# Optimization experiments

Hardware: AMD Instinct MI355X
Metric: run time of the kernel (lower is better)

## Reference

```python
import jax, jax.numpy as jnp
import numpy as np

N = 20000      # nodes
E = 320000     # edges (before self-loops)
F_IN = 512     # input feature size
HID = 128      # encoder hidden
OUT = 128      # encoder output / GAT in_channels
H = 4          # gat heads
C = 64         # gat out_channels per head


def setup_inputs() -> dict:
    key = jax.random.key(0)
    ks = jax.random.split(key, 10)
    s = 0.05
    return {
        "x": jax.random.normal(ks[0], (N, F_IN), jnp.float32),
        "edge_index": jax.random.randint(ks[1], (2, E), 0, N, dtype=jnp.int64),
        "W1": jax.random.normal(ks[2], (F_IN, HID), jnp.float32) * s,
        "b1": jax.random.normal(ks[3], (HID,), jnp.float32) * s,
        "W2": jax.random.normal(ks[4], (HID, OUT), jnp.float32) * s,
        "b2": jax.random.normal(ks[5], (OUT,), jnp.float32) * s,
        "Wg": jax.random.normal(ks[6], (OUT, H * C), jnp.float32) * s,
        "att_src": jax.random.normal(ks[7], (H, C), jnp.float32) * s,
        "att_dst": jax.random.normal(ks[8], (H, C), jnp.float32) * s,
        "bias_g": jax.random.normal(ks[9], (H * C,), jnp.float32) * s,
    }


def reference(x, edge_index, W1, b1, W2, b2, Wg, att_src, att_dst, bias_g):
    # MLP encoder: Linear -> ReLU -> Linear
    h = jnp.maximum(x @ W1 + b1, 0.0) @ W2 + b2            # [N, OUT]

    # GATConv (concat=True, eval mode -> no dropout)
    xg = (h @ Wg).reshape(N, H, C)                          # per-head projections

    # add self-loops (PyG GATConv default)
    loops = jnp.arange(N, dtype=edge_index.dtype)
    src = jnp.concatenate([edge_index[0], loops])           # [E+N] source j
    dst = jnp.concatenate([edge_index[1], loops])           # [E+N] dest   i

    a_src = jnp.einsum('nhc,hc->nh', xg, att_src)           # [N, H]
    a_dst = jnp.einsum('nhc,hc->nh', xg, att_dst)           # [N, H]

    e = jax.nn.leaky_relu(a_src[src] + a_dst[dst], 0.2)     # [E+N, H]

    # segment softmax over incoming edges of each destination node
    m = jax.ops.segment_max(e, dst, num_segments=N)         # [N, H]
    ex = jnp.exp(e - m[dst])
    denom = jax.ops.segment_sum(ex, dst, num_segments=N)
    alpha = ex / (denom[dst] + 1e-16)                       # [E+N, H]

    # weighted scatter-add aggregation
    out = jax.ops.segment_sum(alpha[:, :, None] * xg[src], dst, num_segments=N)  # [N, H, C]
    return out.reshape(N, H * C) + bias_g
```

## Files before the change

kernel.cpp:

```cpp
#include <hip/hip_runtime.h>
#include <math.h>

#define NNODES 20000
#define NEDGES 320000
#define FIN    512
#define HIDD   128
#define OUTD   128
#define NH     4
#define NC     64
#define HC     256

typedef short bf16x8 __attribute__((ext_vector_type(8)));
typedef float f32x4  __attribute__((ext_vector_type(4)));

__device__ __forceinline__ unsigned short f2bf(float f) {
    unsigned int u = __float_as_uint(f);
    unsigned int r = 0x7fffu + ((u >> 16) & 1u);
    return (unsigned short)((u + r) >> 16);
}
__device__ __forceinline__ float bflo(unsigned int u) {
    return __uint_as_float(u << 16);
}
__device__ __forceinline__ float bfhi(unsigned int u) {
    return __uint_as_float(u & 0xffff0000u);
}

#define PREP_TB1 64
#define PREP_TB2 192
__global__ __launch_bounds__(256)
void prep_count_kernel(const float* __restrict__ W1, unsigned short* __restrict__ W1t,
                       const float* __restrict__ W2, const float* __restrict__ b2,
                       const float* __restrict__ Wg, unsigned short* __restrict__ W2gt,
                       float* __restrict__ b2g,
                       const int* __restrict__ e_dst, int* __restrict__ deg, int E) {
    const int bid = blockIdx.x;
    const int tid = threadIdx.x;
    if (bid < PREP_TB1) {
        __shared__ float tile[32][33];
        const int tk = bid >> 2;
        const int tn = bid & 3;
        const int k0 = tk * 32, n0 = tn * 32;
        const int nin = tid & 31;
        const int r8  = tid >> 5;
        #pragma unroll
        for (int s = 0; s < 4; ++s) {
            int k = s * 8 + r8;
            tile[k][nin] = W1[(size_t)(k0 + k) * HIDD + n0 + nin];
        }
        __syncthreads();
        #pragma unroll
        for (int s = 0; s < 4; ++s) {
            int nn = s * 8 + r8;
            W1t[(size_t)(n0 + nn) * FIN + k0 + nin] = f2bf(tile[nin][nn]);
        }
    } else if (bid < PREP_TB2) {
        int local = (bid - PREP_TB1) * 256 + tid;
        int nn = local >> 7;
        int k  = local & 127;
        float s = 0.f;
        #pragma unroll 8
        for (int t = 0; t < HIDD; ++t)
            s += W2[(size_t)k * OUTD + t] * Wg[(size_t)t * HC + nn];
        W2gt[(size_t)nn * HIDD + k] = f2bf(s);
        if (k == 0) {
            float t2 = 0.f;
            #pragma unroll 8
            for (int t = 0; t < OUTD; ++t) t2 += b2[t] * Wg[(size_t)t * HC + nn];
            b2g[nn] = t2;
        }
    } else {
        int i = (bid - PREP_TB2) * 256 + tid;
        if (i < E) atomicAdd(&deg[e_dst[i]], 1);
    }
}

__global__ __launch_bounds__(256)
void gemm1_kernel(const float* __restrict__ A,
                  const unsigned short* __restrict__ Bt,
                  const float* __restrict__ bias,
                  unsigned short* __restrict__ C, int M) {
    __shared__ unsigned short As[32 * 64];
    __shared__ unsigned short Bs[128 * 64];

    const int tid  = threadIdx.x;
    const int lane = tid & 63;
    const int w    = tid >> 6;
    const int wr   = w >> 1;
    const int wc   = w & 1;
    const int m0   = blockIdx.x * 32;

    char* pA = (char*)As;
    char* pB = (char*)Bs;

    f32x4 acc[4];
    #pragma unroll
    for (int n = 0; n < 4; ++n) acc[n] = (f32x4){0.f, 0.f, 0.f, 0.f};

    for (int k0 = 0; k0 < FIN; k0 += 64) {
        {
            const int row = tid >> 3;
            const int sg  = tid & 7;
            const bool ok = (m0 + row) < M;
            const float4* Ap = (const float4*)(A + (size_t)(m0 + row) * FIN + k0 + sg * 8);
            float4 f0 = make_float4(0,0,0,0), f1 = f0;
            if (ok) { f0 = Ap[0]; f1 = Ap[1]; }
            unsigned short u[8];
            u[0]=f2bf(f0.x); u[1]=f2bf(f0.y); u[2]=f2bf(f0.z); u[3]=f2bf(f0.w);
            u[4]=f2bf(f1.x); u[5]=f2bf(f1.y); u[6]=f2bf(f1.z); u[7]=f2bf(f1.w);
            *(bf16x8*)(pA + (((row * 128 + sg * 16)) ^ ((row & 7) << 4))) = *(bf16x8*)&u[0];
        }
        #pragma unroll
        for (int i = 0; i < 4; ++i) {
            int s   = tid + i * 256;
            int col = s >> 3;
            int sg  = s & 7;
            bf16x8 v = *(const bf16x8*)(Bt + (size_t)col * FIN + k0 + sg * 8);
            *(bf16x8*)(pB + (((col * 128 + sg * 16)) ^ ((col & 7) << 4))) = v;
        }
        __syncthreads();

        #pragma unroll
        for (int ks = 0; ks < 2; ++ks) {
            const int kb = ks * 64 + ((lane >> 4) << 4);
            int row = wr * 16 + (lane & 15);
            bf16x8 a = *(const bf16x8*)(pA + ((row * 128 + kb) ^ ((row & 7) << 4)));
            bf16x8 b[4];
            #pragma unroll
            for (int n = 0; n < 4; ++n) {
                int col = wc * 64 + n * 16 + (lane & 15);
                b[n] = *(const bf16x8*)(pB + ((col * 128 + kb) ^ ((col & 7) << 4)));
            }
            #pragma unroll
            for (int n = 0; n < 4; ++n)
                acc[n] = __builtin_amdgcn_mfma_f32_16x16x32_bf16(a, b[n], acc[n], 0, 0, 0);
        }
        __syncthreads();
    }

    #pragma unroll
    for (int n = 0; n < 4; ++n) {
        const int col = wc * 64 + n * 16 + (lane & 15);
        const float bv = bias[col];
        #pragma unroll
        for (int r = 0; r < 4; ++r) {
            const int row = m0 + wr * 16 + ((lane >> 4) << 2) + r;
            if (row >= M) continue;
            float v = fmaxf(acc[n][r] + bv, 0.f);
            C[(size_t)row * HIDD + col] = f2bf(v);
        }
    }
}

__global__ __launch_bounds__(1024)
void scan_offsets_kernel(const int* __restrict__ deg, int* __restrict__ offs,
                         int* __restrict__ cursor, unsigned short* __restrict__ csr16,
                         int n) {
    __shared__ int wsum[16], wbase[16];
    const int tid = threadIdx.x, lane = tid & 63, w = tid >> 6;
    const int i0 = tid * 20;
    int loc[20];
    int s = 0;
    #pragma unroll
    for (int k = 0; k < 20; ++k) {
        int i = i0 + k;
        int v = (i < n) ? (deg[i] + 1) : 0;
        loc[k] = s;
        s += v;
    }
    int incl = s;
    #pragma unroll
    for (int d = 1; d < 64; d <<= 1) {
        int t = __shfl_up(incl, d);
        if (lane >= d) incl += t;
    }
    if (lane == 63) wsum[w] = incl;
    __syncthreads();
    if (w == 0) {
        int v = (lane < 16) ? wsum[lane] : 0;
        int sc = v;
        #pragma unroll
        for (int d = 1; d < 16; d <<= 1) {
            int t = __shfl_up(sc, d);
            if (lane >= d) sc += t;
        }
        if (lane < 16) wbase[lane] = sc - v;
    }
    __syncthreads();
    const int excl = wbase[w] + incl - s;
    #pragma unroll
    for (int k = 0; k < 20; ++k) {
        int i = i0 + k;
        if (i < n) {
            int o = excl + loc[k];
            offs[i]    = o;
            cursor[i]  = o + 1;
            csr16[o]   = (unsigned short)i;
        }
    }
    if (tid == 1023) offs[n] = excl + s;
}

__global__ __launch_bounds__(256)
void gemm2_dots_scatter_kernel(const unsigned short* __restrict__ Ab,
                               const unsigned short* __restrict__ Bt,
                               const float* __restrict__ b2g,
                               const float* __restrict__ att_src,
                               const float* __restrict__ att_dst,
                               unsigned short* __restrict__ xgh,
                               float* __restrict__ a_src,
                               float* __restrict__ a_dst,
                               const int* __restrict__ e_src, const int* __restrict__ e_dst,
                               int* __restrict__ cursor, unsigned short* __restrict__ csr16,
                               int M, int E, int gemmBlocks) {
    const int tid = threadIdx.x;

    if ((int)blockIdx.x >= gemmBlocks) {
        int i = ((int)blockIdx.x - gemmBlocks) * 256 + tid;
        if (i < E) {
            int s = e_src[i], d = e_dst[i];
            csr16[atomicAdd(&cursor[d], 1)] = (unsigned short)s;
        }
        return;
    }

    __shared__ unsigned short As[64 * 64];
    __shared__ unsigned short Bs[128 * 64];

    const int lane = tid & 63;
    const int w    = tid >> 6;
    const int wr   = w >> 1;
    const int wc   = w & 1;
    const int m0   = ((int)blockIdx.x >> 1) * 64;
    const int n0   = ((int)blockIdx.x & 1) * 128;

    char* pA = (char*)As;
    char* pB = (char*)Bs;

    f32x4 acc[2][4];
    #pragma unroll
    for (int m = 0; m < 2; ++m)
        #pragma unroll
        for (int n = 0; n < 4; ++n) acc[m][n] = (f32x4){0.f, 0.f, 0.f, 0.f};

    for (int k0 = 0; k0 < HIDD; k0 += 64) {
        #pragma unroll
        for (int i = 0; i < 2; ++i) {
            int s   = tid + i * 256;
            int row = s >> 3;
            int sg  = s & 7;
            bf16x8 v = {};
            if ((m0 + row) < M)
                v = *(const bf16x8*)(Ab + (size_t)(m0 + row) * HIDD + k0 + sg * 8);
            *(bf16x8*)(pA + (((row * 128 + sg * 16)) ^ ((row & 7) << 4))) = v;
        }
        #pragma unroll
        for (int i = 0; i < 4; ++i) {
            int s   = tid + i * 256;
            int col = s >> 3;
            int sg  = s & 7;
            bf16x8 v = *(const bf16x8*)(Bt + (size_t)(n0 + col) * HIDD + k0 + sg * 8);
            *(bf16x8*)(pB + (((col * 128 + sg * 16)) ^ ((col & 7) << 4))) = v;
        }
        __syncthreads();

        #pragma unroll
        for (int ks = 0; ks < 2; ++ks) {
            const int kb = ks * 64 + ((lane >> 4) << 4);
            bf16x8 a[2], b[4];
            #pragma unroll
            for (int m = 0; m < 2; ++m) {
                int row = wr * 32 + m * 16 + (lane & 15);
                a[m] = *(const bf16x8*)(pA + ((row * 128 + kb) ^ ((row & 7) << 4)));
            }
            #pragma unroll
            for (int n = 0; n < 4; ++n) {
                int col = wc * 64 + n * 16 + (lane & 15);
                b[n] = *(const bf16x8*)(pB + ((col * 128 + kb) ^ ((col & 7) << 4)));
            }
            #pragma unroll
            for (int m = 0; m < 2; ++m)
                #pragma unroll
                for (int n = 0; n < 4; ++n)
                    acc[m][n] = __builtin_amdgcn_mfma_f32_16x16x32_bf16(
                        a[m], b[n], acc[m][n], 0, 0, 0);
        }
        __syncthreads();
    }

    const int head = ((int)blockIdx.x & 1) * 2 + wc;
    const int cIn  = lane & 15;
    unsigned short* plane = xgh + (size_t)head * M * NC;
    float ds_p[2][4], dd_p[2][4];
    #pragma unroll
    for (int m = 0; m < 2; ++m)
        #pragma unroll
        for (int r = 0; r < 4; ++r) { ds_p[m][r] = 0.f; dd_p[m][r] = 0.f; }

    #pragma unroll
    for (int n = 0; n < 4; ++n) {
        const int ch  = n * 16 + cIn;
        const int col = n0 + wc * 64 + n * 16 + cIn;
        const float bv   = b2g[col];
        const float as_c = att_src[head * NC + ch];
        const float ad_c = att_dst[head * NC + ch];
        #pragma unroll
        for (int m = 0; m < 2; ++m) {
            #pragma unroll
            for (int r = 0; r < 4; ++r) {
                const int row = m0 + wr * 32 + m * 16 + ((lane >> 4) << 2) + r;
                float v = acc[m][n][r] + bv;
                if (row < M) plane[(size_t)row * NC + ch] = f2bf(v);
                ds_p[m][r] += v * as_c;
                dd_p[m][r] += v * ad_c;
            }
        }
    }
    #pragma unroll
    for (int m = 0; m < 2; ++m) {
        #pragma unroll
        for (int r = 0; r < 4; ++r) {
            float s = ds_p[m][r], d = dd_p[m][r];
            s += __shfl_xor(s, 1); s += __shfl_xor(s, 2);
            s += __shfl_xor(s, 4); s += __shfl_xor(s, 8);
            d += __shfl_xor(d, 1); d += __shfl_xor(d, 2);
            d += __shfl_xor(d, 4); d += __shfl_xor(d, 8);
            if (cIn == 0) {
                const int row = m0 + wr * 32 + m * 16 + ((lane >> 4) << 2) + r;
                if (row < M) {
                    a_src[(size_t)head * M + row] = s;
                    a_dst[(size_t)head * M + row] = d;
                }
            }
        }
    }
}

__global__ __launch_bounds__(256)
void gat_aggregate7_kernel(const unsigned short* __restrict__ xgh,
                           const float* __restrict__ asrc_h,
                           const float* __restrict__ adst_h,
                           const int* __restrict__ offs,
                           const unsigned short* __restrict__ csr16,
                           const float* __restrict__ bias, float* __restrict__ out,
                           int n, int nbPerHead) {
    const int wv   = threadIdx.x >> 6;
    const int lane = threadIdx.x & 63;
    const int head = (int)blockIdx.x / nbPerHead;
    const int node = ((int)blockIdx.x % nbPerHead) * 4 + wv;
    if (node >= n) return;
    const int g = lane >> 3;
    const int q = lane & 7;
    const int beg = offs[node];
    const int deg = offs[node + 1] - beg;
    const float* asp = asrc_h + (size_t)head * n;
    const float adh = adst_h[(size_t)head * n + node];
    const unsigned short* plane = xgh + (size_t)head * n * NC;

    float acc[8] = {0.f, 0.f, 0.f, 0.f, 0.f, 0.f, 0.f, 0.f};
    float den = 0.f;

    for (int c0 = 0; c0 < deg; c0 += 64) {
        const int j = c0 + lane;
        int   s_l = 0;
        float w_l = 0.f;
        if (j < deg) {
            s_l = csr16[beg + j];
            float e = asp[s_l] + adh;
            e = e > 0.f ? e : 0.2f * e;
            w_l = __expf(e);
        }
        den += w_l;

        const int cn = (deg - c0 < 64) ? (deg - c0) : 64;
        #pragma unroll
        for (int t = 0; t < 8; ++t) {
            if (t * 8 >= cn) break;
            const int jj = t * 8 + g;
            const float wgt = __shfl(w_l, jj);
            const int   s   = __shfl(s_l, jj);
            if (jj < cn) {
                const uint4 u = *(const uint4*)(plane + ((size_t)s << 6) + q * 8);
                acc[0] += wgt * bflo(u.x); acc[1] += wgt * bfhi(u.x);
                acc[2] += wgt * bflo(u.y); acc[3] += wgt * bfhi(u.y);
                acc[4] += wgt * bflo(u.z); acc[5] += wgt * bfhi(u.z);
                acc[6] += wgt * bflo(u.w); acc[7] += wgt * bfhi(u.w);
            }
        }
    }

    #pragma unroll
    for (int mask = 1; mask <= 32; mask <<= 1) den += __shfl_xor(den, mask);
    #pragma unroll
    for (int mask = 8; mask <= 32; mask <<= 1) {
        #pragma unroll
        for (int t = 0; t < 8; ++t) acc[t] += __shfl_xor(acc[t], mask);
    }

    if (g == 0) {
        const float inv = 1.f / (den + 1e-16f);
        const int cb = head * NC + q * 8;
        const int base = node * HC + cb;
        float4 o0 = make_float4(acc[0] * inv + bias[cb + 0],
                                acc[1] * inv + bias[cb + 1],
                                acc[2] * inv + bias[cb + 2],
                                acc[3] * inv + bias[cb + 3]);
        float4 o1 = make_float4(acc[4] * inv + bias[cb + 4],
                                acc[5] * inv + bias[cb + 5],
                                acc[6] * inv + bias[cb + 6],
                                acc[7] * inv + bias[cb + 7]);
        *(float4*)(out + base)     = o0;
        *(float4*)(out + base + 4) = o1;
    }
}

extern "C" void kernel_launch(void* const* d_in, const int* in_sizes, int n_in,
                              void* d_out, int out_size, void* d_ws, size_t ws_size,
                              hipStream_t stream) {
    const float* x       = (const float*)d_in[0];
    const int*   ei      = (const int*)d_in[1];
    const float* W1      = (const float*)d_in[2];
    const float* b1      = (const float*)d_in[3];
    const float* W2      = (const float*)d_in[4];
    const float* b2      = (const float*)d_in[5];
    const float* Wg      = (const float*)d_in[6];
    const float* att_src = (const float*)d_in[7];
    const float* att_dst = (const float*)d_in[8];
    const float* bias_g  = (const float*)d_in[9];

    const int Nn = in_sizes[0] / FIN;
    const int E  = in_sizes[1] / 2;
    const int* e_src = ei;
    const int* e_dst = ei + E;

    char* w = (char*)d_ws;
    auto alloc = [&](size_t bytes) { char* p = w; w += (bytes + 255) & ~(size_t)255; return p; };
    unsigned short* W1t  = (unsigned short*)alloc((size_t)OUTD * FIN * 2);
    unsigned short* W2gt = (unsigned short*)alloc((size_t)HC * HIDD * 2);
    float* b2g  = (float*)alloc(HC * 4);
    unsigned short* h1  = (unsigned short*)alloc((size_t)Nn * HIDD * 2);
    unsigned short* xgh = (unsigned short*)alloc((size_t)NH * Nn * NC * 2);
    float* asrc = (float*)alloc((size_t)NH * Nn * 4);
    float* adst = (float*)alloc((size_t)NH * Nn * 4);
    int* deg    = (int*)alloc((size_t)Nn * 4);
    int* offs   = (int*)alloc((size_t)(Nn + 1) * 4);
    int* cursor = (int*)alloc((size_t)Nn * 4);
    unsigned short* csr16 = (unsigned short*)alloc((size_t)(E + Nn) * 2);

    dim3 blk(256);

    hipMemsetAsync(deg, 0, (size_t)Nn * 4, stream);

    {
        int nb = PREP_TB2 + (E + 255) / 256;
        prep_count_kernel<<<dim3(nb), blk, 0, stream>>>(
            W1, W1t, W2, b2, Wg, W2gt, b2g, e_dst, deg, E);
    }

    gemm1_kernel<<<dim3((Nn + 31) / 32), blk, 0, stream>>>(x, W1t, b1, h1, Nn);

    scan_offsets_kernel<<<dim3(1), dim3(1024), 0, stream>>>(deg, offs, cursor, csr16, Nn);

    {
        int gb = ((Nn + 63) / 64) * 2;
        int sb = (E + 255) / 256;
        gemm2_dots_scatter_kernel<<<dim3(gb + sb), blk, 0, stream>>>(
            h1, W2gt, b2g, att_src, att_dst, xgh, asrc, adst,
            e_src, e_dst, cursor, csr16, Nn, E, gb);
    }

    {
        int nbPerHead = (Nn + 3) / 4;
        gat_aggregate7_kernel<<<dim3(NH * nbPerHead), blk, 0, stream>>>(
            xgh, asrc, adst, offs, csr16, bias_g, (float*)d_out, Nn, nbPerHead);
    }
}
```

Before: 141.8 us.

## Store projected features node-major and aggregate all heads per wavefront

The projected GAT features and attention logits change from a head-planar layout to a node-major one ([N,256] bf16, [N,4] logits). The aggregation kernel now gives each wavefront one node across all four heads, so the CSR neighbour list and the source logits are read once per node instead of once per head. Each lane now gathers 4 channels per edge, 8 edges at a time, with weights and indices staged in shared memory. In exchange each gathered row is 512 bytes, per-lane loads shrink to 8 bytes, and four times fewer blocks are launched.

Result: faster. 127.6 us (-10.1%).

```diff
diff --git a/kernel.cpp b/kernel.cpp
--- a/kernel.cpp
+++ b/kernel.cpp
@@ -206,7 +206,7 @@
                                const float* __restrict__ b2g,
                                const float* __restrict__ att_src,
                                const float* __restrict__ att_dst,
-                               unsigned short* __restrict__ xgh,
+                               unsigned short* __restrict__ xgb,
                                float* __restrict__ a_src,
                                float* __restrict__ a_dst,
                                const int* __restrict__ e_src, const int* __restrict__ e_dst,
@@ -289,7 +289,6 @@
 
     const int head = ((int)blockIdx.x & 1) * 2 + wc;
     const int cIn  = lane & 15;
-    unsigned short* plane = xgh + (size_t)head * M * NC;
     float ds_p[2][4], dd_p[2][4];
     #pragma unroll
     for (int m = 0; m < 2; ++m)
@@ -309,7 +308,7 @@
             for (int r = 0; r < 4; ++r) {
                 const int row = m0 + wr * 32 + m * 16 + ((lane >> 4) << 2) + r;
                 float v = acc[m][n][r] + bv;
-                if (row < M) plane[(size_t)row * NC + ch] = f2bf(v);
+                if (row < M) xgb[(size_t)row * HC + col] = f2bf(v);
                 ds_p[m][r] += v * as_c;
                 dd_p[m][r] += v * ad_c;
             }
@@ -327,8 +326,8 @@
             if (cIn == 0) {
                 const int row = m0 + wr * 32 + m * 16 + ((lane >> 4) << 2) + r;
                 if (row < M) {
-                    a_src[(size_t)head * M + row] = s;
-                    a_dst[(size_t)head * M + row] = d;
+                    a_src[row * NH + head] = s;
+                    a_dst[row * NH + head] = d;
                 }
             }
         }
@@ -336,81 +335,106 @@
 }
 
 __global__ __launch_bounds__(256)
-void gat_aggregate7_kernel(const unsigned short* __restrict__ xgh,
-                           const float* __restrict__ asrc_h,
-                           const float* __restrict__ adst_h,
+void gat_aggregate8_kernel(const unsigned short* __restrict__ xgb,
+                           const float4* __restrict__ asrc4,
+                           const float4* __restrict__ adst4,
                            const int* __restrict__ offs,
                            const unsigned short* __restrict__ csr16,
                            const float* __restrict__ bias, float* __restrict__ out,
-                           int n, int nbPerHead) {
+                           int n) {
+    __shared__ float wbuf[4][4][64];
+    __shared__ int   sbuf[4][64];
     const int wv   = threadIdx.x >> 6;
     const int lane = threadIdx.x & 63;
-    const int head = (int)blockIdx.x / nbPerHead;
-    const int node = ((int)blockIdx.x % nbPerHead) * 4 + wv;
+    const int node = blockIdx.x * 4 + wv;
     if (node >= n) return;
-    const int g = lane >> 3;
-    const int q = lane & 7;
+    const int h = lane >> 4;
     const int beg = offs[node];
     const int deg = offs[node + 1] - beg;
-    const float* asp = asrc_h + (size_t)head * n;
-    const float adh = adst_h[(size_t)head * n + node];
-    const unsigned short* plane = xgh + (size_t)head * n * NC;
-
-    float acc[8] = {0.f, 0.f, 0.f, 0.f, 0.f, 0.f, 0.f, 0.f};
-    float den = 0.f;
+    const float4 adstv = adst4[node];
+
+    float4 den = make_float4(0.f, 0.f, 0.f, 0.f);
+    float4 acc = make_float4(0.f, 0.f, 0.f, 0.f);
 
     for (int c0 = 0; c0 < deg; c0 += 64) {
         const int j = c0 + lane;
         int   s_l = 0;
-        float w_l = 0.f;
+        float4 w4 = make_float4(0.f, 0.f, 0.f, 0.f);
         if (j < deg) {
             s_l = csr16[beg + j];
-            float e = asp[s_l] + adh;
-            e = e > 0.f ? e : 0.2f * e;
-            w_l = __expf(e);
-        }
-        den += w_l;
+            float4 a = asrc4[s_l];
+            float ex_ = a.x + adstv.x, ey = a.y + adstv.y,
+                  ez = a.z + adstv.z, ew = a.w + adstv.w;
+            ex_ = ex_ > 0.f ? ex_ : 0.2f * ex_;
+            ey  = ey  > 0.f ? ey  : 0.2f * ey;
+            ez  = ez  > 0.f ? ez  : 0.2f * ez;
+            ew  = ew  > 0.f ? ew  : 0.2f * ew;
+            w4 = make_float4(__expf(ex_), __expf(ey), __expf(ez), __expf(ew));
+        }
+        den.x += w4.x; den.y += w4.y; den.z += w4.z; den.w += w4.w;
+        sbuf[wv][lane]    = s_l;
+        wbuf[wv][0][lane] = w4.x;
+        wbuf[wv][1][lane] = w4.y;
+        wbuf[wv][2][lane] = w4.z;
+        wbuf[wv][3][lane] = w4.w;
 
         const int cn = (deg - c0 < 64) ? (deg - c0) : 64;
-        #pragma unroll
-        for (int t = 0; t < 8; ++t) {
-            if (t * 8 >= cn) break;
-            const int jj = t * 8 + g;
-            const float wgt = __shfl(w_l, jj);
-            const int   s   = __shfl(s_l, jj);
-            if (jj < cn) {
-                const uint4 u = *(const uint4*)(plane + ((size_t)s << 6) + q * 8);
-                acc[0] += wgt * bflo(u.x); acc[1] += wgt * bfhi(u.x);
-                acc[2] += wgt * bflo(u.y); acc[3] += wgt * bfhi(u.y);
-                acc[4] += wgt * bflo(u.z); acc[5] += wgt * bfhi(u.z);
-                acc[6] += wgt * bflo(u.w); acc[7] += wgt * bfhi(u.w);
-            }
-        }
-    }
-
-    #pragma unroll
-    for (int mask = 1; mask <= 32; mask <<= 1) den += __shfl_xor(den, mask);
-    #pragma unroll
-    for (int mask = 8; mask <= 32; mask <<= 1) {
-        #pragma unroll
-        for (int t = 0; t < 8; ++t) acc[t] += __shfl_xor(acc[t], mask);
-    }
-
-    if (g == 0) {
-        const float inv = 1.f / (den + 1e-16f);
-        const int cb = head * NC + q * 8;
-        const int base = node * HC + cb;
-        float4 o0 = make_float4(acc[0] * inv + bias[cb + 0],
-                                acc[1] * inv + bias[cb + 1],
-                                acc[2] * inv + bias[cb + 2],
-                                acc[3] * inv + bias[cb + 3]);
-        float4 o1 = make_float4(acc[4] * inv + bias[cb + 4],
-                                acc[5] * inv + bias[cb + 5],
-                                acc[6] * inv + bias[cb + 6],
-                                acc[7] * inv + bias[cb + 7]);
-        *(float4*)(out + base)     = o0;
-        *(float4*)(out + base + 4) = o1;
-    }
+        const size_t chbase = (size_t)lane * 4;
+        int jj = 0;
+        for (; jj + 8 <= cn; jj += 8) {
+            float wg[8]; int ss[8]; uint2 uu[8];
+            #pragma unroll
+            for (int t = 0; t < 8; ++t) {
+                wg[t] = wbuf[wv][h][jj + t];
+                ss[t] = sbuf[wv][jj + t];
+            }
+            #pragma unroll
+            for (int t = 0; t < 8; ++t)
+                uu[t] = *(const uint2*)(xgb + (size_t)ss[t] * HC + chbase);
+            #pragma unroll
+            for (int t = 0; t < 8; ++t) {
+                acc.x += wg[t] * bflo(uu[t].x);
+                acc.y += wg[t] * bfhi(uu[t].x);
+                acc.z += wg[t] * bflo(uu[t].y);
+                acc.w += wg[t] * bfhi(uu[t].y);
+            }
+        }
+        if (jj < cn) {
+            float wg[8]; int ss[8]; uint2 uu[8];
+            #pragma unroll
+            for (int t = 0; t < 8; ++t) {
+                int je = jj + t;
+                bool ok = je < cn;
+                wg[t] = ok ? wbuf[wv][h][je] : 0.f;
+                ss[t] = sbuf[wv][ok ? je : 0];
+            }
+            #pragma unroll
+            for (int t = 0; t < 8; ++t)
+                uu[t] = *(const uint2*)(xgb + (size_t)ss[t] * HC + chbase);
+            #pragma unroll
+            for (int t = 0; t < 8; ++t) {
+                acc.x += wg[t] * bflo(uu[t].x);
+                acc.y += wg[t] * bfhi(uu[t].x);
+                acc.z += wg[t] * bflo(uu[t].y);
+                acc.w += wg[t] * bfhi(uu[t].y);
+            }
+        }
+    }
+
+    #pragma unroll
+    for (int mask = 1; mask <= 32; mask <<= 1) {
+        den.x += __shfl_xor(den.x, mask);
+        den.y += __shfl_xor(den.y, mask);
+        den.z += __shfl_xor(den.z, mask);
+        den.w += __shfl_xor(den.w, mask);
+    }
+    const float denh = (h == 0) ? den.x : (h == 1) ? den.y : (h == 2) ? den.z : den.w;
+    const float inv = 1.f / (denh + 1e-16f);
+
+    const float4 bv = ((const float4*)bias)[lane];
+    float4 o = make_float4(acc.x * inv + bv.x, acc.y * inv + bv.y,
+                           acc.z * inv + bv.z, acc.w * inv + bv.w);
+    ((float4*)out)[(size_t)node * 64 + lane] = o;
 }
 
 extern "C" void kernel_launch(void* const* d_in, const int* in_sizes, int n_in,
@@ -438,9 +462,9 @@
     unsigned short* W2gt = (unsigned short*)alloc((size_t)HC * HIDD * 2);
     float* b2g  = (float*)alloc(HC * 4);
     unsigned short* h1  = (unsigned short*)alloc((size_t)Nn * HIDD * 2);
-    unsigned short* xgh = (unsigned short*)alloc((size_t)NH * Nn * NC * 2);
-    float* asrc = (float*)alloc((size_t)NH * Nn * 4);
-    float* adst = (float*)alloc((size_t)NH * Nn * 4);
+    unsigned short* xgb = (unsigned short*)alloc((size_t)Nn * HC * 2);
+    float* asrc = (float*)alloc((size_t)Nn * NH * 4);
+    float* adst = (float*)alloc((size_t)Nn * NH * 4);
     int* deg    = (int*)alloc((size_t)Nn * 4);
     int* offs   = (int*)alloc((size_t)(Nn + 1) * 4);
     int* cursor = (int*)alloc((size_t)Nn * 4);
@@ -464,13 +488,11 @@
         int gb = ((Nn + 63) / 64) * 2;
         int sb = (E + 255) / 256;
         gemm2_dots_scatter_kernel<<<dim3(gb + sb), blk, 0, stream>>>(
-            h1, W2gt, b2g, att_src, att_dst, xgh, asrc, adst,
+            h1, W2gt, b2g, att_src, att_dst, xgb, asrc, adst,
             e_src, e_dst, cursor, csr16, Nn, E, gb);
     }
 
-    {
-        int nbPerHead = (Nn + 3) / 4;
-        gat_aggregate7_kernel<<<dim3(NH * nbPerHead), blk, 0, stream>>>(
-            xgh, asrc, adst, offs, csr16, bias_g, (float*)d_out, Nn, nbPerHead);
-    }
-}
+    gat_aggregate8_kernel<<<dim3((Nn + 3) / 4), blk, 0, stream>>>(
+        xgb, (const float4*)asrc, (const float4*)adst, offs, csr16, bias_g,
+        (float*)d_out, Nn);
+}
```
